# Kernel tuning notes

Hardware: AMD Instinct MI355X
Metric: run time of the kernel (lower is better)

## Reference

```python
import jax, jax.numpy as jnp
import numpy as np

HID = 128
CDIM = 128
NCH = 3
NDIM = 3


def _linear_params(key, fan_in, fan_out):
    kw, kb = jax.random.split(key)
    bound = 1.0 / np.sqrt(fan_in)
    W = jax.random.uniform(kw, (fan_in, fan_out), jnp.float32, -bound, bound)
    b = jax.random.uniform(kb, (fan_out,), jnp.float32, -bound, bound)
    return W, b


def setup_inputs() -> dict:
    key = jax.random.key(0)
    keys = jax.random.split(key, 12)
    p = jax.random.normal(keys[0], (32, 8192, NDIM), jnp.float32)
    W_pos, b_pos = _linear_params(keys[1], NDIM, 2 * HID)
    W0, b0 = _linear_params(keys[2], 2 * HID, HID)
    W1, b1 = _linear_params(keys[3], 2 * HID, HID)
    W2, b2 = _linear_params(keys[4], 2 * HID, HID)
    W3, b3 = _linear_params(keys[5], 2 * HID, HID)
    Wc, bc = _linear_params(keys[6], HID, CDIM)
    Wm0, bm0 = _linear_params(keys[7], CDIM, HID)
    Wm1, bm1 = _linear_params(keys[8], HID, HID)
    Wm2, bm2 = _linear_params(keys[9], HID, HID)
    Wp, bp = _linear_params(keys[10], HID, NCH * 3)
    return dict(p=p, W_pos=W_pos, b_pos=b_pos, W0=W0, b0=b0, W1=W1, b1=b1,
                W2=W2, b2=b2, W3=W3, b3=b3, Wc=Wc, bc=bc,
                Wm0=Wm0, bm0=bm0, Wm1=Wm1, bm1=bm1, Wm2=Wm2, bm2=bm2,
                Wp=Wp, bp=bp)


def _relu(x):
    return jnp.maximum(x, 0)


def _pool_cat(net):
    # max over points (dim=1), broadcast back and concat on features
    pooled = jnp.max(net, axis=1, keepdims=True)
    pooled = jnp.broadcast_to(pooled, net.shape)
    return jnp.concatenate([net, pooled], axis=2)  # [B, T, 2*hid]


def reference(p, W_pos, b_pos, W0, b0, W1, b1, W2, b2, W3, b3,
              Wc, bc, Wm0, bm0, Wm1, bm1, Wm2, bm2, Wp, bp):
    net = p @ W_pos + b_pos                      # [B, T, 2*hid]
    net = _relu(net) @ W0 + b0                   # [B, T, hid]
    net = _relu(_pool_cat(net)) @ W1 + b1        # [B, T, hid]
    net = _relu(_pool_cat(net)) @ W2 + b2        # [B, T, hid]
    net = _relu(_pool_cat(net)) @ W3 + b3        # [B, T, hid]
    net = jnp.max(net, axis=1)                   # [B, hid]
    net = _relu(net) @ Wc + bc                   # [B, c_dim]
    net = _relu(net) @ Wm0 + bm0
    net = _relu(net) @ Wm1 + bm1
    net = _relu(net) @ Wm2 + bm2
    net = _relu(net) @ Wp + bp                   # [B, n_channels*3]
    return net
```

## Files before the change

### kernel.cpp

```cpp
#include <hip/hip_runtime.h>


using bf16x8 = __attribute__((ext_vector_type(8))) __bf16;
using u16x8  = __attribute__((ext_vector_type(8))) unsigned short;
using f32x4  = __attribute__((ext_vector_type(4))) float;

__device__ __forceinline__ unsigned short f2bf(float x) {
  __bf16 b = (__bf16)x;
  return __builtin_bit_cast(unsigned short, b);
}

__device__ __forceinline__ f32x4 mfma16(bf16x8 a, bf16x8 b, f32x4 c) {
  return __builtin_amdgcn_mfma_f32_16x16x32_bf16(a, b, c, 0, 0, 0);
}

union FragU { unsigned short us[8]; u16x8 u; bf16x8 v; };

__global__ __launch_bounds__(256) void k_pack_all(
    const float* __restrict__ W0, const float* __restrict__ W1,
    const float* __restrict__ W2, const float* __restrict__ W3,
    unsigned short* __restrict__ Wt) {
  const int blk = blockIdx.x, t = threadIdx.x;
  const float* src; int slot; unsigned short* dst;
  if (blk < 16)      { src = W0; slot = blk * 256 + t;        dst = Wt; }
  else if (blk < 24) { src = W1; slot = (blk - 16) * 256 + t; dst = Wt + 32768; }
  else if (blk < 32) { src = W2; slot = (blk - 24) * 256 + t; dst = Wt + 49152; }
  else               { src = W3; slot = (blk - 32) * 256 + t; dst = Wt + 65536; }
  const int ks = slot >> 9, rem = slot & 511;
  const int nt = rem >> 6, lane = rem & 63;
  const int n = nt * 16 + (lane & 15);
  const int kb = ks * 32 + ((lane >> 4) << 3);
  FragU fr;
#pragma unroll
  for (int j = 0; j < 8; ++j) fr.us[j] = f2bf(src[(kb + j) * 128 + n]);
  reinterpret_cast<u16x8*>(dst)[slot] = fr.u;
}

__global__ __launch_bounds__(256) void k_layer0(
    const float* __restrict__ p, const float* __restrict__ Wpos,
    const float* __restrict__ bpos, const float* __restrict__ b0,
    const unsigned short* __restrict__ Wt0, unsigned short* __restrict__ h,
    float* __restrict__ pm) {
  __shared__ float wls[1024];
  __shared__ unsigned short Afrag[16384];
  __shared__ float pmaxs[2][128];
  const int t = threadIdx.x, blk = blockIdx.x;
  for (int i = t; i < 1024; i += 256) wls[i] = (i < 768) ? Wpos[i] : bpos[i - 768];

  const int w = t >> 6, lane = t & 63, g = lane >> 4, c = lane & 15;

  float px[4], py[4], pz[4];
#pragma unroll
  for (int tl = 0; tl < 4; ++tl) {
    const int row = blk * 64 + tl * 16 + c;
    px[tl] = p[row * 3 + 0]; py[tl] = p[row * 3 + 1]; pz[tl] = p[row * 3 + 2];
  }
  __syncthreads();

#pragma unroll
  for (int i = 0; i < 8; ++i) {
    const int tl = i & 3;
    const int ks = w * 2 + (i >> 2);
    const int kb = ks * 32 + g * 8;
    FragU fr;
#pragma unroll
    for (int j = 0; j < 8; ++j) {
      const int k = kb + j;
      fr.us[j] = f2bf(fmaxf(wls[768 + k] + px[tl] * wls[k] + py[tl] * wls[256 + k] + pz[tl] * wls[512 + k], 0.f));
    }
    *reinterpret_cast<u16x8*>(&Afrag[((tl * 8 + ks) * 64 + lane) * 8]) = fr.u;
  }
  __syncthreads();

  const int rowg = w >> 1, colg = w & 1;
  f32x4 acc[2][4];
#pragma unroll
  for (int mi = 0; mi < 2; ++mi)
#pragma unroll
    for (int ntl = 0; ntl < 4; ++ntl) acc[mi][ntl] = f32x4{0.f, 0.f, 0.f, 0.f};

  const bf16x8* Bf = reinterpret_cast<const bf16x8*>(Wt0);
  const u16x8* Af = reinterpret_cast<const u16x8*>(Afrag);
#pragma unroll
  for (int ks = 0; ks < 8; ++ks) {
    bf16x8 B[4];
#pragma unroll
    for (int ntl = 0; ntl < 4; ++ntl)
      B[ntl] = Bf[(ks * 8 + colg * 4 + ntl) * 64 + lane];
    FragU a0, a1;
    a0.u = Af[((rowg * 2 + 0) * 8 + ks) * 64 + lane];
    a1.u = Af[((rowg * 2 + 1) * 8 + ks) * 64 + lane];
#pragma unroll
    for (int ntl = 0; ntl < 4; ++ntl) {
      acc[0][ntl] = mfma16(B[ntl], a0.v, acc[0][ntl]);
      acc[1][ntl] = mfma16(B[ntl], a1.v, acc[1][ntl]);
    }
  }

  unsigned short* hout = h + (size_t)blk * 8192;
#pragma unroll
  for (int ntl = 0; ntl < 4; ++ntl) {
    const int ntg = colg * 4 + ntl;
    const float4 bb = *reinterpret_cast<const float4*>(&b0[ntg * 16 + g * 4]);
    float vm[4] = {0.f, 0.f, 0.f, 0.f};
#pragma unroll
    for (int mi = 0; mi < 2; ++mi) {
      const float v0 = fmaxf(acc[mi][ntl][0] + bb.x, 0.f);
      const float v1 = fmaxf(acc[mi][ntl][1] + bb.y, 0.f);
      const float v2 = fmaxf(acc[mi][ntl][2] + bb.z, 0.f);
      const float v3 = fmaxf(acc[mi][ntl][3] + bb.w, 0.f);
      vm[0] = fmaxf(vm[0], v0); vm[1] = fmaxf(vm[1], v1);
      vm[2] = fmaxf(vm[2], v2); vm[3] = fmaxf(vm[3], v3);
      ushort4 s4;
      s4.x = f2bf(v0); s4.y = f2bf(v1); s4.z = f2bf(v2); s4.w = f2bf(v3);
      const int slot = (rowg * 2 + mi) * 256 + (ntg >> 1) * 64 +
                       ((ntg & 1) * 2 + (g >> 1)) * 16 + c;
      *reinterpret_cast<ushort4*>(&hout[slot * 8 + (g & 1) * 4]) = s4;
    }
#pragma unroll
    for (int r = 0; r < 4; ++r) {
      vm[r] = fmaxf(vm[r], __shfl_xor(vm[r], 1, 64));
      vm[r] = fmaxf(vm[r], __shfl_xor(vm[r], 2, 64));
      vm[r] = fmaxf(vm[r], __shfl_xor(vm[r], 4, 64));
      vm[r] = fmaxf(vm[r], __shfl_xor(vm[r], 8, 64));
    }
    if (c == 0) {
#pragma unroll
      for (int r = 0; r < 4; ++r) pmaxs[rowg][ntg * 16 + g * 4 + r] = vm[r];
    }
  }
  __syncthreads();
  if (t < 128) pm[(size_t)blk * 128 + t] = fmaxf(pmaxs[0][t], pmaxs[1][t]);
}

__global__ __launch_bounds__(256) void k_layer(
    const unsigned short* __restrict__ Wta, const float* __restrict__ cvec,
    unsigned short* __restrict__ h, float* __restrict__ pm, int write_h) {
  __shared__ float pmaxs[2][128];
  const int t = threadIdx.x, blk = blockIdx.x;
  const int w = t >> 6, lane = t & 63, g = lane >> 4, c = lane & 15;
  const int rowg = w >> 1, colg = w & 1;
  const int b = blk >> 6;

  f32x4 acc[4][4];
#pragma unroll
  for (int mi = 0; mi < 4; ++mi)
#pragma unroll
    for (int ntl = 0; ntl < 4; ++ntl) acc[mi][ntl] = f32x4{0.f, 0.f, 0.f, 0.f};

  const u16x8* hblk = reinterpret_cast<const u16x8*>(h) + (size_t)blk * 2048;
  const bf16x8* Bf = reinterpret_cast<const bf16x8*>(Wta);
#pragma unroll
  for (int ks = 0; ks < 4; ++ks) {
    bf16x8 B[4];
#pragma unroll
    for (int ntl = 0; ntl < 4; ++ntl)
      B[ntl] = Bf[(ks * 8 + colg * 4 + ntl) * 64 + lane];
    FragU a[4];
#pragma unroll
    for (int mi = 0; mi < 4; ++mi)
      a[mi].u = hblk[(rowg * 4 + mi) * 256 + ks * 64 + lane];
#pragma unroll
    for (int mi = 0; mi < 4; ++mi)
#pragma unroll
      for (int ntl = 0; ntl < 4; ++ntl)
        acc[mi][ntl] = mfma16(B[ntl], a[mi].v, acc[mi][ntl]);
  }

  unsigned short* hout = h + (size_t)blk * 16384;
  const float* biasvec = cvec + b * 128;
#pragma unroll
  for (int ntl = 0; ntl < 4; ++ntl) {
    const int ntg = colg * 4 + ntl;
    const float4 bb = *reinterpret_cast<const float4*>(&biasvec[ntg * 16 + g * 4]);
    float vm[4] = {0.f, 0.f, 0.f, 0.f};
#pragma unroll
    for (int mi = 0; mi < 4; ++mi) {
      const float v0 = fmaxf(acc[mi][ntl][0] + bb.x, 0.f);
      const float v1 = fmaxf(acc[mi][ntl][1] + bb.y, 0.f);
      const float v2 = fmaxf(acc[mi][ntl][2] + bb.z, 0.f);
      const float v3 = fmaxf(acc[mi][ntl][3] + bb.w, 0.f);
      vm[0] = fmaxf(vm[0], v0); vm[1] = fmaxf(vm[1], v1);
      vm[2] = fmaxf(vm[2], v2); vm[3] = fmaxf(vm[3], v3);
      if (write_h) {
        ushort4 s4;
        s4.x = f2bf(v0); s4.y = f2bf(v1); s4.z = f2bf(v2); s4.w = f2bf(v3);
        const int slot = (rowg * 4 + mi) * 256 + (ntg >> 1) * 64 +
                         ((ntg & 1) * 2 + (g >> 1)) * 16 + c;
        *reinterpret_cast<ushort4*>(&hout[slot * 8 + (g & 1) * 4]) = s4;
      }
    }
#pragma unroll
    for (int r = 0; r < 4; ++r) {
      vm[r] = fmaxf(vm[r], __shfl_xor(vm[r], 1, 64));
      vm[r] = fmaxf(vm[r], __shfl_xor(vm[r], 2, 64));
      vm[r] = fmaxf(vm[r], __shfl_xor(vm[r], 4, 64));
      vm[r] = fmaxf(vm[r], __shfl_xor(vm[r], 8, 64));
    }
    if (c == 0) {
#pragma unroll
      for (int r = 0; r < 4; ++r) pmaxs[rowg][ntg * 16 + g * 4 + r] = vm[r];
    }
  }
  __syncthreads();
  if (t < 128) pm[(size_t)blk * 128 + t] = fmaxf(pmaxs[0][t], pmaxs[1][t]);
}

__global__ __launch_bounds__(256) void k_combine(
    const float* __restrict__ pm, const float* __restrict__ Wn,
    const float* __restrict__ bn, float* __restrict__ cout, int nper) {
  const int b = blockIdx.x, t = threadIdx.x;
  const int f = t & 127, half = t >> 7;
  __shared__ float part[2][128];
  __shared__ float rm[128];
  const int hn = nper >> 1;
  float m = 0.f;
  for (int i = half * hn; i < half * hn + hn; ++i)
    m = fmaxf(m, pm[(size_t)(b * nper + i) * 128 + f]);
  part[half][f] = m;
  __syncthreads();
  if (t < 128) rm[f] = fmaxf(part[0][f], part[1][f]);
  __syncthreads();
  float s = 0.f;
  for (int q = half * 64; q < half * 64 + 64; ++q)
    s += rm[q] * Wn[(128 + q) * 128 + f];
  part[half][f] = s;
  __syncthreads();
  if (t < 128) cout[b * 128 + f] = part[0][f] + part[1][f] + bn[f];
}

__global__ __launch_bounds__(256) void k_final(
    const float* __restrict__ pm3, int nper,
    const float* __restrict__ Wc,  const float* __restrict__ bc,
    const float* __restrict__ Wm0, const float* __restrict__ bm0,
    const float* __restrict__ Wm1, const float* __restrict__ bm1,
    const float* __restrict__ Wm2, const float* __restrict__ bm2,
    const float* __restrict__ Wp,  const float* __restrict__ bp,
    float* __restrict__ out) {
  const int b = blockIdx.x, t = threadIdx.x;
  const int f = t & 127, half = t >> 7;
  __shared__ float part[2][128];
  __shared__ float x[128];
  const int hn = nper >> 1;
  float m = 0.f;
  for (int i = half * hn; i < half * hn + hn; ++i)
    m = fmaxf(m, pm3[(size_t)(b * nper + i) * 128 + f]);
  part[half][f] = m;
  __syncthreads();
  if (t < 128) x[f] = fmaxf(part[0][f], part[1][f]);
  __syncthreads();

  const float* Ws[4] = {Wc, Wm0, Wm1, Wm2};
  const float* bs[4] = {bc, bm0, bm1, bm2};
#pragma unroll
  for (int L = 0; L < 4; ++L) {
    float s = 0.f;
    for (int q = half * 64; q < half * 64 + 64; ++q)
      s += x[q] * Ws[L][q * 128 + f];
    part[half][f] = s;
    __syncthreads();
    if (t < 128) x[f] = fmaxf(part[0][f] + part[1][f] + bs[L][f], 0.f);
    __syncthreads();
  }
  if (t < 9) {
    float s = bp[t];
    for (int q = 0; q < 128; ++q) s += x[q] * Wp[q * 9 + t];
    out[b * 9 + t] = s;
  }
}

extern "C" void kernel_launch(void* const* d_in, const int* in_sizes, int n_in,
                              void* d_out, int out_size, void* d_ws, size_t ws_size,
                              hipStream_t stream) {
  const float *p = nullptr, *Wpos = nullptr, *bpos = nullptr;
  const float *Wp = nullptr, *bp = nullptr;
  const float *W256[4] = {}; int nW256 = 0;
  const float *W128[4] = {}; int nW128 = 0;
  const float *B128[8] = {}; int nB128 = 0;
  for (int i = 0; i < n_in; ++i) {
    const float* q = (const float*)d_in[i];
    switch (in_sizes[i]) {
      case 786432: p = q; break;
      case 768:    Wpos = q; break;
      case 256:    bpos = q; break;
      case 1152:   Wp = q; break;
      case 9:      bp = q; break;
      case 32768:  if (nW256 < 4) W256[nW256++] = q; break;
      case 16384:  if (nW128 < 4) W128[nW128++] = q; break;
      case 128:    if (nB128 < 8) B128[nB128++] = q; break;
      default: break;
    }
  }
  const float *W0 = W256[0], *W1 = W256[1], *W2 = W256[2], *W3 = W256[3];
  const float *Wc = W128[0], *Wm0 = W128[1], *Wm1 = W128[2], *Wm2 = W128[3];
  const float *b0 = B128[0], *b1 = B128[1], *b2 = B128[2], *b3 = B128[3];
  const float *bc = B128[4], *bm0 = B128[5], *bm1 = B128[6], *bm2 = B128[7];
  float* out = (float*)d_out;

  char* ws = (char*)d_ws;
  float* pm = (float*)ws;
  float* cv = (float*)(ws + 2097152);
  unsigned short* Wt = (unsigned short*)(ws + 2097152 + 16384);
  unsigned short* Wt0 = Wt;
  unsigned short* Wt1 = Wt + 32768;
  unsigned short* Wt2 = Wt + 49152;
  unsigned short* Wt3 = Wt + 65536;
  unsigned short* h = Wt + 81920;

  k_pack_all<<<40, 256, 0, stream>>>(W0, W1, W2, W3, Wt);
  k_layer0<<<4096, 256, 0, stream>>>(p, Wpos, bpos, b0, Wt0, h, pm);
  k_combine<<<32, 256, 0, stream>>>(pm, W1, b1, cv, 128);
  k_layer<<<2048, 256, 0, stream>>>(Wt1, cv, h, pm, 1);
  k_combine<<<32, 256, 0, stream>>>(pm, W2, b2, cv, 64);
  k_layer<<<2048, 256, 0, stream>>>(Wt2, cv, h, pm, 1);
  k_combine<<<32, 256, 0, stream>>>(pm, W3, b3, cv, 64);
  k_layer<<<2048, 256, 0, stream>>>(Wt3, cv, h, pm, 0);
  k_final<<<32, 256, 0, stream>>>(pm, 64, Wc, bc, Wm0, bm0, Wm1, bm1, Wm2, bm2, Wp, bp, out);
}
```

Measured before the change: 194.0 us.

## Fuse pooled-bias combine into layer kernels and compute pos-embedding via MFMA

```diff
diff --git a/kernel.cpp b/kernel.cpp
--- a/kernel.cpp
+++ b/kernel.cpp
@@ -41,38 +41,60 @@
     const float* __restrict__ bpos, const float* __restrict__ b0,
     const unsigned short* __restrict__ Wt0, unsigned short* __restrict__ h,
     float* __restrict__ pm) {
-  __shared__ float wls[1024];
-  __shared__ unsigned short Afrag[16384];
+  __shared__ unsigned short wlsb[1024];
   __shared__ float pmaxs[2][128];
   const int t = threadIdx.x, blk = blockIdx.x;
-  for (int i = t; i < 1024; i += 256) wls[i] = (i < 768) ? Wpos[i] : bpos[i - 768];
+
+  {
+    const int m = t;
+    const int phi = ((m >> 4) >> 1) * 32 + (((m & 15) >> 2) << 3) +
+                    (((m >> 4) & 1) << 2) + (m & 3);
+    ushort4 wv;
+    wv.x = f2bf(Wpos[phi]);       wv.y = f2bf(Wpos[256 + phi]);
+    wv.z = f2bf(Wpos[512 + phi]); wv.w = f2bf(bpos[phi]);
+    *reinterpret_cast<ushort4*>(&wlsb[m * 4]) = wv;
+  }
+  __syncthreads();
 
   const int w = t >> 6, lane = t & 63, g = lane >> 4, c = lane & 15;
-
-  float px[4], py[4], pz[4];
-#pragma unroll
-  for (int tl = 0; tl < 4; ++tl) {
-    const int row = blk * 64 + tl * 16 + c;
-    px[tl] = p[row * 3 + 0]; py[tl] = p[row * 3 + 1]; pz[tl] = p[row * 3 + 2];
-  }
-  __syncthreads();
-
-#pragma unroll
-  for (int i = 0; i < 8; ++i) {
-    const int tl = i & 3;
-    const int ks = w * 2 + (i >> 2);
-    const int kb = ks * 32 + g * 8;
-    FragU fr;
-#pragma unroll
-    for (int j = 0; j < 8; ++j) {
-      const int k = kb + j;
-      fr.us[j] = f2bf(fmaxf(wls[768 + k] + px[tl] * wls[k] + py[tl] * wls[256 + k] + pz[tl] * wls[512 + k], 0.f));
-    }
-    *reinterpret_cast<u16x8*>(&Afrag[((tl * 8 + ks) * 64 + lane) * 8]) = fr.u;
-  }
-  __syncthreads();
-
   const int rowg = w >> 1, colg = w & 1;
+
+  FragU pf[2];
+#pragma unroll
+  for (int mi = 0; mi < 2; ++mi) {
+#pragma unroll
+    for (int j = 0; j < 8; ++j) pf[mi].us[j] = 0;
+    const int row = blk * 64 + rowg * 32 + mi * 16 + c;
+    if (g == 0) {
+      pf[mi].us[0] = f2bf(p[row * 3 + 0]);
+      pf[mi].us[1] = f2bf(p[row * 3 + 1]);
+      pf[mi].us[2] = f2bf(p[row * 3 + 2]);
+      pf[mi].us[3] = (unsigned short)0x3F80;
+    }
+  }
+
+  FragU af[2][8];
+#pragma unroll
+  for (int mi = 0; mi < 2; ++mi) {
+    f32x4 qe[16];
+#pragma unroll
+    for (int nt = 0; nt < 16; ++nt) {
+      FragU a1;
+#pragma unroll
+      for (int j = 0; j < 8; ++j) a1.us[j] = 0;
+      if (g == 0) {
+        const ushort4 wv = *reinterpret_cast<const ushort4*>(&wlsb[(nt * 16 + c) * 4]);
+        a1.us[0] = wv.x; a1.us[1] = wv.y; a1.us[2] = wv.z; a1.us[3] = wv.w;
+      }
+      qe[nt] = mfma16(a1.v, pf[mi].v, f32x4{0.f, 0.f, 0.f, 0.f});
+    }
+#pragma unroll
+    for (int ks = 0; ks < 8; ++ks)
+#pragma unroll
+      for (int j = 0; j < 8; ++j)
+        af[mi][ks].us[j] = f2bf(fmaxf(qe[ks * 2 + (j >> 2)][j & 3], 0.f));
+  }
+
   f32x4 acc[2][4];
 #pragma unroll
   for (int mi = 0; mi < 2; ++mi)
@@ -80,20 +102,13 @@
     for (int ntl = 0; ntl < 4; ++ntl) acc[mi][ntl] = f32x4{0.f, 0.f, 0.f, 0.f};
 
   const bf16x8* Bf = reinterpret_cast<const bf16x8*>(Wt0);
-  const u16x8* Af = reinterpret_cast<const u16x8*>(Afrag);
 #pragma unroll
   for (int ks = 0; ks < 8; ++ks) {
-    bf16x8 B[4];
-#pragma unroll
-    for (int ntl = 0; ntl < 4; ++ntl)
-      B[ntl] = Bf[(ks * 8 + colg * 4 + ntl) * 64 + lane];
-    FragU a0, a1;
-    a0.u = Af[((rowg * 2 + 0) * 8 + ks) * 64 + lane];
-    a1.u = Af[((rowg * 2 + 1) * 8 + ks) * 64 + lane];
 #pragma unroll
     for (int ntl = 0; ntl < 4; ++ntl) {
-      acc[0][ntl] = mfma16(B[ntl], a0.v, acc[0][ntl]);
-      acc[1][ntl] = mfma16(B[ntl], a1.v, acc[1][ntl]);
+      const bf16x8 B = Bf[(ks * 8 + colg * 4 + ntl) * 64 + lane];
+      acc[0][ntl] = mfma16(B, af[0][ks].v, acc[0][ntl]);
+      acc[1][ntl] = mfma16(B, af[1][ks].v, acc[1][ntl]);
     }
   }
 
@@ -134,13 +149,33 @@
 }
 
 __global__ __launch_bounds__(256) void k_layer(
-    const unsigned short* __restrict__ Wta, const float* __restrict__ cvec,
-    unsigned short* __restrict__ h, float* __restrict__ pm, int write_h) {
+    const unsigned short* __restrict__ Wta, const float* __restrict__ Wn,
+    const float* __restrict__ bn, const float* __restrict__ pmin, int nper,
+    unsigned short* __restrict__ h, float* __restrict__ pmout, int write_h) {
+  __shared__ float part[2][128];
+  __shared__ float rm[128];
+  __shared__ float cvv[128];
   __shared__ float pmaxs[2][128];
   const int t = threadIdx.x, blk = blockIdx.x;
   const int w = t >> 6, lane = t & 63, g = lane >> 4, c = lane & 15;
   const int rowg = w >> 1, colg = w & 1;
   const int b = blk >> 6;
+  const int f = t & 127, half = t >> 7, hn = nper >> 1;
+
+  float m = 0.f;
+  for (int i = half * hn; i < half * hn + hn; ++i)
+    m = fmaxf(m, pmin[(size_t)(b * nper + i) * 128 + f]);
+  part[half][f] = m;
+  __syncthreads();
+  if (t < 128) rm[f] = fmaxf(part[0][f], part[1][f]);
+  __syncthreads();
+  float s = 0.f;
+  for (int q = half * 64; q < half * 64 + 64; ++q)
+    s += rm[q] * Wn[(128 + q) * 128 + f];
+  part[half][f] = s;
+  __syncthreads();
+  if (t < 128) cvv[f] = part[0][f] + part[1][f] + bn[f];
+  __syncthreads();
 
   f32x4 acc[4][4];
 #pragma unroll
@@ -168,11 +203,10 @@
   }
 
   unsigned short* hout = h + (size_t)blk * 16384;
-  const float* biasvec = cvec + b * 128;
 #pragma unroll
   for (int ntl = 0; ntl < 4; ++ntl) {
     const int ntg = colg * 4 + ntl;
-    const float4 bb = *reinterpret_cast<const float4*>(&biasvec[ntg * 16 + g * 4]);
+    const float4 bb = *reinterpret_cast<const float4*>(&cvv[ntg * 16 + g * 4]);
     float vm[4] = {0.f, 0.f, 0.f, 0.f};
 #pragma unroll
     for (int mi = 0; mi < 4; ++mi) {
@@ -203,30 +237,7 @@
     }
   }
   __syncthreads();
-  if (t < 128) pm[(size_t)blk * 128 + t] = fmaxf(pmaxs[0][t], pmaxs[1][t]);
-}
-
-__global__ __launch_bounds__(256) void k_combine(
-    const float* __restrict__ pm, const float* __restrict__ Wn,
-    const float* __restrict__ bn, float* __restrict__ cout, int nper) {
-  const int b = blockIdx.x, t = threadIdx.x;
-  const int f = t & 127, half = t >> 7;
-  __shared__ float part[2][128];
-  __shared__ float rm[128];
-  const int hn = nper >> 1;
-  float m = 0.f;
-  for (int i = half * hn; i < half * hn + hn; ++i)
-    m = fmaxf(m, pm[(size_t)(b * nper + i) * 128 + f]);
-  part[half][f] = m;
-  __syncthreads();
-  if (t < 128) rm[f] = fmaxf(part[0][f], part[1][f]);
-  __syncthreads();
-  float s = 0.f;
-  for (int q = half * 64; q < half * 64 + 64; ++q)
-    s += rm[q] * Wn[(128 + q) * 128 + f];
-  part[half][f] = s;
-  __syncthreads();
-  if (t < 128) cout[b * 128 + f] = part[0][f] + part[1][f] + bn[f];
+  if (t < 128) pmout[(size_t)blk * 128 + t] = fmaxf(pmaxs[0][t], pmaxs[1][t]);
 }
 
 __global__ __launch_bounds__(256) void k_final(
@@ -298,9 +309,9 @@
   float* out = (float*)d_out;
 
   char* ws = (char*)d_ws;
-  float* pm = (float*)ws;
-  float* cv = (float*)(ws + 2097152);
-  unsigned short* Wt = (unsigned short*)(ws + 2097152 + 16384);
+  float* pm0 = (float*)ws;
+  float* pm1 = (float*)(ws + 2097152);
+  unsigned short* Wt = (unsigned short*)(ws + 3145728);
   unsigned short* Wt0 = Wt;
   unsigned short* Wt1 = Wt + 32768;
   unsigned short* Wt2 = Wt + 49152;
@@ -308,12 +319,9 @@
   unsigned short* h = Wt + 81920;
 
   k_pack_all<<<40, 256, 0, stream>>>(W0, W1, W2, W3, Wt);
-  k_layer0<<<4096, 256, 0, stream>>>(p, Wpos, bpos, b0, Wt0, h, pm);
-  k_combine<<<32, 256, 0, stream>>>(pm, W1, b1, cv, 128);
-  k_layer<<<2048, 256, 0, stream>>>(Wt1, cv, h, pm, 1);
-  k_combine<<<32, 256, 0, stream>>>(pm, W2, b2, cv, 64);
-  k_layer<<<2048, 256, 0, stream>>>(Wt2, cv, h, pm, 1);
-  k_combine<<<32, 256, 0, stream>>>(pm, W3, b3, cv, 64);
-  k_layer<<<2048, 256, 0, stream>>>(Wt3, cv, h, pm, 0);
-  k_final<<<32, 256, 0, stream>>>(pm, 64, Wc, bc, Wm0, bm0, Wm1, bm1, Wm2, bm2, Wp, bp, out);
-}
+  k_layer0<<<4096, 256, 0, stream>>>(p, Wpos, bpos, b0, Wt0, h, pm0);
+  k_layer<<<2048, 256, 0, stream>>>(Wt1, W1, b1, pm0, 128, h, pm1, 1);
+  k_layer<<<2048, 256, 0, stream>>>(Wt2, W2, b2, pm1, 64, h, pm0, 1);
+  k_layer<<<2048, 256, 0, stream>>>(Wt3, W3, b3, pm0, 64, h, pm1, 0);
+  k_final<<<32, 256, 0, stream>>>(pm1, 64, Wc, bc, Wm0, bm0, Wm1, bm1, Wm2, bm2, Wp, bp, out);
+}
```

Measured after the change: 301.4 us. 1.55x slower.

## Compute layer-0 position embedding with MFMA instead of scalar FMAs and LDS staging

Applied to the files above, without the earlier changes.

```diff
diff --git a/kernel.cpp b/kernel.cpp
--- a/kernel.cpp
+++ b/kernel.cpp
@@ -41,38 +41,38 @@
     const float* __restrict__ bpos, const float* __restrict__ b0,
     const unsigned short* __restrict__ Wt0, unsigned short* __restrict__ h,
     float* __restrict__ pm) {
-  __shared__ float wls[1024];
-  __shared__ unsigned short Afrag[16384];
+  __shared__ unsigned short wlsb[1024];
   __shared__ float pmaxs[2][128];
   const int t = threadIdx.x, blk = blockIdx.x;
-  for (int i = t; i < 1024; i += 256) wls[i] = (i < 768) ? Wpos[i] : bpos[i - 768];
+
+  {
+    const int m = t;
+    const int phi = ((m >> 4) >> 1) * 32 + (((m & 15) >> 2) << 3) +
+                    (((m >> 4) & 1) << 2) + (m & 3);
+    ushort4 wv;
+    wv.x = f2bf(Wpos[phi]);       wv.y = f2bf(Wpos[256 + phi]);
+    wv.z = f2bf(Wpos[512 + phi]); wv.w = f2bf(bpos[phi]);
+    *reinterpret_cast<ushort4*>(&wlsb[m * 4]) = wv;
+  }
+  __syncthreads();
 
   const int w = t >> 6, lane = t & 63, g = lane >> 4, c = lane & 15;
-
-  float px[4], py[4], pz[4];
-#pragma unroll
-  for (int tl = 0; tl < 4; ++tl) {
-    const int row = blk * 64 + tl * 16 + c;
-    px[tl] = p[row * 3 + 0]; py[tl] = p[row * 3 + 1]; pz[tl] = p[row * 3 + 2];
-  }
-  __syncthreads();
-
-#pragma unroll
-  for (int i = 0; i < 8; ++i) {
-    const int tl = i & 3;
-    const int ks = w * 2 + (i >> 2);
-    const int kb = ks * 32 + g * 8;
-    FragU fr;
-#pragma unroll
-    for (int j = 0; j < 8; ++j) {
-      const int k = kb + j;
-      fr.us[j] = f2bf(fmaxf(wls[768 + k] + px[tl] * wls[k] + py[tl] * wls[256 + k] + pz[tl] * wls[512 + k], 0.f));
-    }
-    *reinterpret_cast<u16x8*>(&Afrag[((tl * 8 + ks) * 64 + lane) * 8]) = fr.u;
-  }
-  __syncthreads();
-
   const int rowg = w >> 1, colg = w & 1;
+
+  FragU pf[2];
+#pragma unroll
+  for (int mi = 0; mi < 2; ++mi) {
+#pragma unroll
+    for (int j = 0; j < 8; ++j) pf[mi].us[j] = 0;
+    if (g == 0) {
+      const int row = blk * 64 + rowg * 32 + mi * 16 + c;
+      pf[mi].us[0] = f2bf(p[row * 3 + 0]);
+      pf[mi].us[1] = f2bf(p[row * 3 + 1]);
+      pf[mi].us[2] = f2bf(p[row * 3 + 2]);
+      pf[mi].us[3] = (unsigned short)0x3F80;
+    }
+  }
+
   f32x4 acc[2][4];
 #pragma unroll
   for (int mi = 0; mi < 2; ++mi)
@@ -80,20 +80,37 @@
     for (int ntl = 0; ntl < 4; ++ntl) acc[mi][ntl] = f32x4{0.f, 0.f, 0.f, 0.f};
 
   const bf16x8* Bf = reinterpret_cast<const bf16x8*>(Wt0);
-  const u16x8* Af = reinterpret_cast<const u16x8*>(Afrag);
+  const f32x4 zz = {0.f, 0.f, 0.f, 0.f};
+
 #pragma unroll
   for (int ks = 0; ks < 8; ++ks) {
     bf16x8 B[4];
 #pragma unroll
     for (int ntl = 0; ntl < 4; ++ntl)
       B[ntl] = Bf[(ks * 8 + colg * 4 + ntl) * 64 + lane];
-    FragU a0, a1;
-    a0.u = Af[((rowg * 2 + 0) * 8 + ks) * 64 + lane];
-    a1.u = Af[((rowg * 2 + 1) * 8 + ks) * 64 + lane];
-#pragma unroll
-    for (int ntl = 0; ntl < 4; ++ntl) {
-      acc[0][ntl] = mfma16(B[ntl], a0.v, acc[0][ntl]);
-      acc[1][ntl] = mfma16(B[ntl], a1.v, acc[1][ntl]);
+
+    FragU a1_0, a1_1;
+#pragma unroll
+    for (int j = 0; j < 8; ++j) { a1_0.us[j] = 0; a1_1.us[j] = 0; }
+    if (g == 0) {
+      const ushort4 wv0 = *reinterpret_cast<const ushort4*>(&wlsb[((2 * ks) * 16 + c) * 4]);
+      const ushort4 wv1 = *reinterpret_cast<const ushort4*>(&wlsb[((2 * ks + 1) * 16 + c) * 4]);
+      a1_0.us[0] = wv0.x; a1_0.us[1] = wv0.y; a1_0.us[2] = wv0.z; a1_0.us[3] = wv0.w;
+      a1_1.us[0] = wv1.x; a1_1.us[1] = wv1.y; a1_1.us[2] = wv1.z; a1_1.us[3] = wv1.w;
+    }
+
+#pragma unroll
+    for (int mi = 0; mi < 2; ++mi) {
+      const f32x4 qe0 = mfma16(a1_0.v, pf[mi].v, zz);
+      const f32x4 qe1 = mfma16(a1_1.v, pf[mi].v, zz);
+      FragU af;
+#pragma unroll
+      for (int j = 0; j < 4; ++j) af.us[j] = f2bf(fmaxf(qe0[j], 0.f));
+#pragma unroll
+      for (int j = 0; j < 4; ++j) af.us[4 + j] = f2bf(fmaxf(qe1[j], 0.f));
+#pragma unroll
+      for (int ntl = 0; ntl < 4; ++ntl)
+        acc[mi][ntl] = mfma16(B[ntl], af.v, acc[mi][ntl]);
     }
   }
 
@@ -168,11 +185,10 @@
   }
 
   unsigned short* hout = h + (size_t)blk * 16384;
-  const float* biasvec = cvec + b * 128;
 #pragma unroll
   for (int ntl = 0; ntl < 4; ++ntl) {
     const int ntg = colg * 4 + ntl;
-    const float4 bb = *reinterpret_cast<const float4*>(&biasvec[ntg * 16 + g * 4]);
+    const float4 bb = *reinterpret_cast<const float4*>(&cvec[b * 128 + ntg * 16 + g * 4]);
     float vm[4] = {0.f, 0.f, 0.f, 0.f};
 #pragma unroll
     for (int mi = 0; mi < 4; ++mi) {
```

After: 179.9 us. -7.3%, faster.
